# Performance work log

Hardware: AMD Instinct MI355X
Metric: run time of the kernel (lower is better)

## Reference

```python
import jax, jax.numpy as jnp
import numpy as np

HIDDEN = 1024
NUM_TOTAL = 8
NUM_SHARED = 2
NUM_ROUTED = NUM_TOTAL - NUM_SHARED
TOP_K = 2
TOKENS = 16384
SCALE = 0.02


def setup_inputs() -> dict:
    key = jax.random.key(0)
    ks = jax.random.split(key, 12)
    h = HIDDEN
    inp = {
        "x": jax.random.normal(ks[0], (TOKENS, h), dtype=jnp.float32),
        # shared experts: [E_s, in, hidden] / [E_s, hidden] etc. (y = x @ W + b)
        "shared_w1": jax.random.normal(ks[1], (NUM_SHARED, h, h), jnp.float32) * SCALE,
        "shared_b1": jnp.zeros((NUM_SHARED, h), jnp.float32),
        "shared_w2": jax.random.normal(ks[2], (NUM_SHARED, h, h), jnp.float32) * SCALE,
        "shared_b2": jnp.zeros((NUM_SHARED, h), jnp.float32),
        # routed experts
        "routed_w1": jax.random.normal(ks[3], (NUM_ROUTED, h, h), jnp.float32) * SCALE,
        "routed_b1": jnp.zeros((NUM_ROUTED, h), jnp.float32),
        "routed_w2": jax.random.normal(ks[4], (NUM_ROUTED, h, h), jnp.float32) * SCALE,
        "routed_b2": jnp.zeros((NUM_ROUTED, h), jnp.float32),
        # router: Linear(hidden, num_routed)
        "router_w": jax.random.normal(ks[5], (h, NUM_ROUTED), jnp.float32) * SCALE,
        "router_b": jnp.zeros((NUM_ROUTED,), jnp.float32),
    }
    return inp


def _expert_all(x, w1, b1, w2, b2):
    # x: [B, H]; w1/w2: [E, H, H]; returns [B, E, H]
    hmid = jnp.tanh(jnp.einsum("bi,eio->beo", x, w1) + b1)
    return jnp.einsum("beh,eho->beo", hmid, w2) + b2


def reference(x, shared_w1, shared_b1, shared_w2, shared_b2,
              routed_w1, routed_b1, routed_w2, routed_b2,
              router_w, router_b):
    # shared experts: every token through every shared expert, summed
    shared_out = _expert_all(x, shared_w1, shared_b1, shared_w2, shared_b2).sum(axis=1)  # [B,H]

    # router softmax + top-k mask (original weights each expert by
    # routing_weights[:, i] * mask[:, i], i.e. NOT renormalized)
    logits = x @ router_w + router_b                       # [B, E_r]
    routing_weights = jax.nn.softmax(logits, axis=-1)      # [B, E_r]
    _, top_idx = jax.lax.top_k(routing_weights, TOP_K)     # [B, k]
    mask = jax.nn.one_hot(top_idx, NUM_ROUTED, dtype=routing_weights.dtype).sum(axis=1)  # [B, E_r]
    weight = routing_weights * mask                        # [B, E_r]

    # dense all-expert compute masked by top-k (faithful to source loop)
    expert_out = _expert_all(x, routed_w1, routed_b1, routed_w2, routed_b2)  # [B, E_r, H]
    routed_out = jnp.einsum("be,beh->bh", weight, expert_out)

    return shared_out + routed_out
```

## Files before the change

### kernel.cpp

```cpp
#include <hip/hip_runtime.h>
#include <hip/hip_bf16.h>

#define H 1024
#define B_TOK 16384
#define RTILES 262
#define RCAP   (RTILES * 128)

typedef __attribute__((ext_vector_type(8))) short s16x8;
typedef __attribute__((ext_vector_type(4))) float f32x4;

__device__ __forceinline__ short f2bf(float f) {
  __hip_bfloat16 h = __float2bfloat16(f);
  return __builtin_bit_cast(short, h);
}
__device__ __forceinline__ float bf2f(short s) {
  __hip_bfloat16 h = __builtin_bit_cast(__hip_bfloat16, s);
  return __bfloat162float(h);
}

__device__ __forceinline__ void load_lds16(const short* g, short* l) {
  __builtin_amdgcn_global_load_lds((const __attribute__((address_space(1))) void*)g,
                                   (__attribute__((address_space(3))) void*)l,
                                   16, 0, 0);
}

__global__ void cvt_x_k(const float* __restrict__ x, short* __restrict__ xb) {
  const size_t i = ((size_t)blockIdx.x * blockDim.x + threadIdx.x) * 8;
  const float4 a = *(const float4*)(x + i);
  const float4 b = *(const float4*)(x + i + 4);
  s16x8 v;
  v[0] = f2bf(a.x); v[1] = f2bf(a.y); v[2] = f2bf(a.z); v[3] = f2bf(a.w);
  v[4] = f2bf(b.x); v[5] = f2bf(b.y); v[6] = f2bf(b.z); v[7] = f2bf(b.w);
  *(s16x8*)(xb + i) = v;
}

__global__ void transpose_k(const float* __restrict__ sw1, const float* __restrict__ rw1,
                            const float* __restrict__ sw2, const float* __restrict__ rw2,
                            short* __restrict__ w1t, short* __restrict__ w2t_sh,
                            short* __restrict__ w2t_r) {
  __shared__ float tile[64][65];
  const int z = blockIdx.z;
  const float* src;
  short* dst;
  int ldd = H, koff = 0;
  if (z < 8) {
    src = (z < 2) ? sw1 + (size_t)z * H * H : rw1 + (size_t)(z - 2) * H * H;
    dst = w1t + (size_t)z * H * H;
  } else if (z < 10) {
    const int e = z - 8;
    src = sw2 + (size_t)e * H * H;
    dst = w2t_sh; ldd = 2048; koff = e * 1024;
  } else {
    const int e = z - 10;
    src = rw2 + (size_t)e * H * H;
    dst = w2t_r + (size_t)e * H * H;
  }
  const int k0 = blockIdx.y * 64, n0 = blockIdx.x * 64;
  const int t = threadIdx.x;
#pragma unroll
  for (int i = 0; i < 4; ++i) {
    const int kk = (t >> 4) + 16 * i;
    const int nn = (t & 15) * 4;
    const float4 v = *(const float4*)(src + (size_t)(k0 + kk) * H + n0 + nn);
    tile[nn + 0][kk] = v.x; tile[nn + 1][kk] = v.y;
    tile[nn + 2][kk] = v.z; tile[nn + 3][kk] = v.w;
  }
  __syncthreads();
  const int nn = t >> 2;
  const int kk = (t & 3) * 16;
  s16x8 o0, o1;
#pragma unroll
  for (int u = 0; u < 8; ++u) {
    o0[u] = f2bf(tile[nn][kk + u]);
    o1[u] = f2bf(tile[nn][kk + 8 + u]);
  }
  short* drow = dst + (size_t)(n0 + nn) * ldd + koff + k0 + kk;
  *(s16x8*)(drow) = o0;
  *(s16x8*)(drow + 8) = o1;
}

__global__ void logits_k(const float* __restrict__ x, const float* __restrict__ rw,
                         const float* __restrict__ rb, int2* __restrict__ tk) {
  const int lane = threadIdx.x & 63;
  const int b = blockIdx.x * 4 + (threadIdx.x >> 6);
  const float* xr = x + (size_t)b * H;
  float p[6] = {0.f, 0.f, 0.f, 0.f, 0.f, 0.f};
  for (int k = lane; k < H; k += 64) {
    const float xv = xr[k];
    const float* r = rw + k * 6;
#pragma unroll
    for (int e = 0; e < 6; ++e) p[e] += xv * r[e];
  }
#pragma unroll
  for (int e = 0; e < 6; ++e) {
    float v = p[e];
    for (int off = 32; off > 0; off >>= 1) v += __shfl_down(v, off);
    p[e] = v;
  }
  if (lane == 0) {
    float lg[6];
    float mx = -1e30f;
#pragma unroll
    for (int e = 0; e < 6; ++e) { lg[e] = p[e] + rb[e]; mx = fmaxf(mx, lg[e]); }
    float s = 0.f;
#pragma unroll
    for (int e = 0; e < 6; ++e) { lg[e] = __expf(lg[e] - mx); s += lg[e]; }
    const float inv = 1.f / s;
#pragma unroll
    for (int e = 0; e < 6; ++e) lg[e] *= inv;
    int i1 = 0;
#pragma unroll
    for (int e = 1; e < 6; ++e) if (lg[e] > lg[i1]) i1 = e;
    int i2 = (i1 == 0) ? 1 : 0;
#pragma unroll
    for (int e = 0; e < 6; ++e) if (e != i1 && lg[e] > lg[i2]) i2 = e;
    int2 v;
    v.x = i1 | ((int)(unsigned short)f2bf(lg[i1]) << 16);
    v.y = i2 | ((int)(unsigned short)f2bf(lg[i2]) << 16);
    tk[b] = v;
  }
}

__global__ void hist_k(const int2* __restrict__ tk, int* __restrict__ g) {
  __shared__ int h[6];
  const int t = threadIdx.x;
  if (t < 6) h[t] = 0;
  __syncthreads();
  const int2 v = tk[blockIdx.x * 256 + t];
  atomicAdd(&h[v.x & 0xffff], 1);
  atomicAdd(&h[v.y & 0xffff], 1);
  __syncthreads();
  if (t < 6) atomicAdd(&g[t], h[t]);
}

__global__ void prefix_k(int* __restrict__ g) {
  if (threadIdx.x == 0) {
    int run = 0;
#pragma unroll
    for (int e = 0; e < 6; ++e) {
      g[8 + e] = run; g[16 + e] = run;
      run += (g[e] + 127) & ~127;
    }
    g[14] = run;
  }
}

__global__ void scatter_k(const int2* __restrict__ tk, int* __restrict__ g,
                          int* __restrict__ asg) {
  __shared__ int lcnt[6];
  __shared__ int lbase[6];
  const int t = threadIdx.x;
  if (t < 6) lcnt[t] = 0;
  __syncthreads();
  const int tok = blockIdx.x * 256 + t;
  const int2 v = tk[tok];
  const int e1 = v.x & 0xffff, e2 = v.y & 0xffff;
  const int p1 = atomicAdd(&lcnt[e1], 1);
  const int p2 = atomicAdd(&lcnt[e2], 1);
  __syncthreads();
  if (t < 6) lbase[t] = atomicAdd(&g[16 + t], lcnt[t]);
  __syncthreads();
  asg[lbase[e1] + p1] = tok | (v.x & 0xffff0000);
  asg[lbase[e2] + p2] = tok | (v.y & 0xffff0000);
}

__device__ __forceinline__ void gemm_core64(const short* __restrict__ A, int lda,
                                            const short* __restrict__ Bt, int ldb, int K,
                                            short* smem, int m0, int n0,
                                            const int* __restrict__ asg, int acap,
                                            f32x4 acc[4][4]) {
  const int tid = threadIdx.x, lane = tid & 63, w = tid >> 6;
  const int q8 = (lane >> 4) * 8, r16 = lane & 15;
  const int wr = w >> 1, wc = w & 1;

  const short* gp[4];
#pragma unroll
  for (int ii = 0; ii < 4; ++ii) {
    const int c2 = w * 4 + ii;
    if (c2 < 8) {
      int slot = m0 + c2 * 16 + r16;
      int gr;
      if (asg) {
        int tv = asg[slot] & 0xffff;
        gr = tv < B_TOK ? tv : B_TOK - 1;
      } else {
        gr = slot < acap ? slot : acap - 1;
      }
      gp[ii] = A + (size_t)gr * lda + q8;
    } else {
      gp[ii] = Bt + (size_t)(n0 + (c2 - 8) * 16 + r16) * ldb + q8;
    }
  }
  short* lbase = smem + w * 4096;

  for (int k0 = 0; k0 < K; k0 += 64) {
    __syncthreads();
#pragma unroll
    for (int i = 0; i < 8; ++i)
      load_lds16(gp[i >> 1] + k0 + (i & 1) * 32, lbase + i * 512);
    __syncthreads();
#pragma unroll
    for (int s = 0; s < 2; ++s) {
      s16x8 af[4], bfv[4];
#pragma unroll
      for (int i = 0; i < 4; ++i)
        af[i] = *(const s16x8*)(smem + ((wr * 4 + i) * 2 + s) * 512 + lane * 8);
#pragma unroll
      for (int j = 0; j < 4; ++j)
        bfv[j] = *(const s16x8*)(smem + (16 + (wc * 4 + j) * 2 + s) * 512 + lane * 8);
#pragma unroll
      for (int i = 0; i < 4; ++i)
#pragma unroll
        for (int j = 0; j < 4; ++j)
          acc[i][j] = __builtin_amdgcn_mfma_f32_16x16x32_bf16(af[i], bfv[j], acc[i][j], 0, 0, 0);
    }
  }
}

template <int ROUTED>
__global__ __launch_bounds__(256) void gemm1_k(const short* __restrict__ A, int lda,
                                               const short* __restrict__ W1, int ldb, int K,
                                               const float* __restrict__ b1,
                                               short* __restrict__ Out, int ldo,
                                               const int* __restrict__ asg,
                                               const int* __restrict__ g, int rowcap) {
  const int m0 = blockIdx.x * 128, n0 = blockIdx.y * 128;
  const short* Bt = W1;
  const float* bias = b1;
  if (ROUTED) {
    if (m0 >= g[14]) return;
    int e = 0;
#pragma unroll
    for (int j = 1; j < 6; ++j) if (m0 >= g[8 + j]) e = j;
    Bt = W1 + (size_t)e * H * H;
    bias = b1 + (size_t)e * H;
  }
  __shared__ __align__(16) short smem[16384];
  f32x4 acc[4][4];
#pragma unroll
  for (int i = 0; i < 4; ++i)
#pragma unroll
    for (int j = 0; j < 4; ++j) acc[i][j] = (f32x4){0.f, 0.f, 0.f, 0.f};
  gemm_core64(A, lda, Bt, ldb, K, smem, m0, n0, ROUTED ? asg : nullptr, 1 << 30, acc);

  const int tid = threadIdx.x, lane = tid & 63, w = tid >> 6;
  const int wr = w >> 1, wc = w & 1, q = lane >> 4, c16 = lane & 15;
  __syncthreads();
#pragma unroll
  for (int j = 0; j < 4; ++j) {
    const int colL = wc * 64 + j * 16 + c16;
    const float bv = bias[n0 + colL];
#pragma unroll
    for (int i = 0; i < 4; ++i)
#pragma unroll
      for (int r = 0; r < 4; ++r)
        smem[(wr * 64 + i * 16 + q * 4 + r) * 128 + colL] = f2bf(tanhf(acc[i][j][r] + bv));
  }
  __syncthreads();
#pragma unroll
  for (int p = 0; p < 8; ++p) {
    const int rowL = p * 16 + (tid >> 4);
    const int colL = (tid & 15) * 8;
    const int gr = m0 + rowL;
    if (gr < rowcap)
      *(s16x8*)(Out + (size_t)gr * ldo + n0 + colL) = *(const s16x8*)(smem + rowL * 128 + colL);
  }
}

template <int MODE>
__global__ __launch_bounds__(256) void gemm2_k(const short* __restrict__ A, int lda,
                                               const short* __restrict__ W2, int ldb, int K,
                                               const float* __restrict__ b2a,
                                               const float* __restrict__ b2b,
                                               float* __restrict__ Out,
                                               const int* __restrict__ asg,
                                               const int* __restrict__ g, int acap) {
  const int m0 = blockIdx.x * 128, n0 = blockIdx.y * 128;
  const short* Bt = W2;
  const float* bias = b2a;
  if (MODE == 3) {
    if (m0 >= g[14]) return;
    int e = 0;
#pragma unroll
    for (int j = 1; j < 6; ++j) if (m0 >= g[8 + j]) e = j;
    Bt = W2 + (size_t)e * H * H;
    bias = b2a + (size_t)e * H;
  }
  __shared__ __align__(16) short smem[16384];
  f32x4 acc[4][4];
#pragma unroll
  for (int i = 0; i < 4; ++i)
#pragma unroll
    for (int j = 0; j < 4; ++j) acc[i][j] = (f32x4){0.f, 0.f, 0.f, 0.f};
  gemm_core64(A, lda, Bt, ldb, K, smem, m0, n0, nullptr, acap, acc);

  const int tid = threadIdx.x, lane = tid & 63, w = tid >> 6;
  const int wr = w >> 1, wc = w & 1, q = lane >> 4, c16 = lane & 15;

  if (MODE == 0) {
    float* cs = (float*)smem;
    __syncthreads();
#pragma unroll
    for (int half = 0; half < 2; ++half) {
      if (wr == half) {
#pragma unroll
        for (int j = 0; j < 4; ++j) {
          const int colL = wc * 64 + j * 16 + c16;
          const float bv = b2a[n0 + colL] + b2b[n0 + colL];
#pragma unroll
          for (int i = 0; i < 4; ++i)
#pragma unroll
            for (int r = 0; r < 4; ++r)
              cs[(i * 16 + q * 4 + r) * 128 + colL] = acc[i][j][r] + bv;
        }
      }
      __syncthreads();
#pragma unroll
      for (int p = 0; p < 8; ++p) {
        const int rowL = p * 8 + (tid >> 5);
        const int colL = (tid & 31) * 4;
        *(float4*)(Out + (size_t)(m0 + half * 64 + rowL) * H + n0 + colL) =
            *(const float4*)(cs + rowL * 128 + colL);
      }
      __syncthreads();
    }
  } else {
    const int mb = m0 + wr * 64, nb = n0 + wc * 64;
#pragma unroll
    for (int i = 0; i < 4; ++i) {
      int av[4];
#pragma unroll
      for (int r = 0; r < 4; ++r) av[r] = asg[mb + i * 16 + q * 4 + r];
#pragma unroll
      for (int j = 0; j < 4; ++j) {
        const int col = nb + j * 16 + c16;
        const float bv = bias[col];
#pragma unroll
        for (int r = 0; r < 4; ++r) {
          if (av[r] == -1) continue;
          const int tok = av[r] & 0xffff;
          const float wt = bf2f((short)((unsigned)av[r] >> 16));
          atomicAdd(&Out[(size_t)tok * H + col], (acc[i][j][r] + bv) * wt);
        }
      }
    }
  }
}

extern "C" void kernel_launch(void* const* d_in, const int* in_sizes, int n_in,
                              void* d_out, int out_size, void* d_ws, size_t ws_size,
                              hipStream_t stream) {
  const float* x        = (const float*)d_in[0];
  const float* sw1      = (const float*)d_in[1];
  const float* sb1      = (const float*)d_in[2];
  const float* sw2      = (const float*)d_in[3];
  const float* sb2      = (const float*)d_in[4];
  const float* rw1      = (const float*)d_in[5];
  const float* rb1      = (const float*)d_in[6];
  const float* rw2      = (const float*)d_in[7];
  const float* rb2      = (const float*)d_in[8];
  const float* router_w = (const float*)d_in[9];
  const float* router_b = (const float*)d_in[10];
  float* out = (float*)d_out;

  char* ws = (char*)d_ws;
  short* xb     = (short*)(ws);
  short* w1t    = (short*)(ws + (size_t)33554432);
  short* w2t_r  = (short*)(ws + (size_t)50331648);
  short* w2t_sh = (short*)(ws + (size_t)62914560);
  short* hm_sh  = (short*)(ws + (size_t)67108864);
  short* hm_r   = (short*)(ws + (size_t)62914560);
  int2*  tk     = (int2*)hm_sh;
  int*   g      = (int*)(ws + (size_t)134217728);
  int*   asg    = (int*)(ws + (size_t)134217984);

  hipMemsetAsync(g, 0, 64, stream);
  hipMemsetAsync(asg, 0xFF, RCAP * sizeof(int), stream);

  cvt_x_k<<<8192, 256, 0, stream>>>(x, xb);
  transpose_k<<<dim3(16, 16, 16), 256, 0, stream>>>(sw1, rw1, sw2, rw2, w1t, w2t_sh, w2t_r);
  logits_k<<<4096, 256, 0, stream>>>(x, router_w, router_b, tk);
  hist_k<<<64, 256, 0, stream>>>(tk, g);
  prefix_k<<<1, 64, 0, stream>>>(g);
  scatter_k<<<64, 256, 0, stream>>>(tk, g, asg);

  gemm1_k<0><<<dim3(128, 16), 256, 0, stream>>>(xb, H, w1t, H, H, sb1, hm_sh, 2048,
                                                nullptr, nullptr, 1 << 30);
  gemm2_k<0><<<dim3(128, 8), 256, 0, stream>>>(hm_sh, 2048, w2t_sh, 2048, 2048,
                                               sb2, sb2 + H, out, nullptr, nullptr, 1 << 30);

  gemm1_k<1><<<dim3(RTILES, 8), 256, 0, stream>>>(xb, H, w1t + (size_t)2 * H * H, H, H,
                                                  rb1, hm_r, H, asg, g, RCAP);
  gemm2_k<3><<<dim3(RTILES, 8), 256, 0, stream>>>(hm_r, H, w2t_r, H, H,
                                                  rb2, nullptr, out, asg, g, RCAP);
}
```

Measured before the change: 834.1 us.

## Remap GEMM tiles across XCDs, use fast tanh, raise occupancy hint

The GEMM grids become one-dimensional and each block index is remapped so that consecutive tiles land on the same XCD (an 8-way chiplet-aware swizzle), which should improve L2 reuse of A rows and weight columns. Row-major tile ordering within an XCD keeps N tiles of one M stripe together. The tanh epilogue switches from tanhf to an exp/fast-divide formula. Launch bounds now request 6 waves per SIMD, which may force register spilling. The fast tanh is less accurate and can produce NaN for large inputs when exp overflows to inf, though 2/inf gives 0, so it should stay safe.

```diff
diff --git a/kernel.cpp b/kernel.cpp
--- a/kernel.cpp
+++ b/kernel.cpp
@@ -18,10 +18,25 @@
   return __bfloat162float(h);
 }
 
+__device__ __forceinline__ float fast_tanh(float x) {
+  const float e = __expf(2.f * x);
+  return 1.f - __fdividef(2.f, e + 1.f);
+}
+
 __device__ __forceinline__ void load_lds16(const short* g, short* l) {
   __builtin_amdgcn_global_load_lds((const __attribute__((address_space(1))) void*)g,
                                    (__attribute__((address_space(3))) void*)l,
                                    16, 0, 0);
+}
+
+template <int NY>
+__device__ __forceinline__ void tile_coords128(int& m0, int& n0) {
+  const int nwg = gridDim.x, o = blockIdx.x;
+  const int q = nwg >> 3, r = nwg & 7;
+  const int x = o & 7, oo = o >> 3;
+  const int wg = (x < r ? x * (q + 1) : r * (q + 1) + (x - r) * q) + oo;
+  m0 = (wg / NY) * 128;
+  n0 = (wg % NY) * 128;
 }
 
 __global__ void cvt_x_k(const float* __restrict__ x, short* __restrict__ xb) {
@@ -217,14 +232,15 @@
   }
 }
 
-template <int ROUTED>
-__global__ __launch_bounds__(256) void gemm1_k(const short* __restrict__ A, int lda,
-                                               const short* __restrict__ W1, int ldb, int K,
-                                               const float* __restrict__ b1,
-                                               short* __restrict__ Out, int ldo,
-                                               const int* __restrict__ asg,
-                                               const int* __restrict__ g, int rowcap) {
-  const int m0 = blockIdx.x * 128, n0 = blockIdx.y * 128;
+template <int ROUTED, int NY>
+__global__ __launch_bounds__(256, 6) void gemm1_k(const short* __restrict__ A, int lda,
+                                                  const short* __restrict__ W1, int ldb, int K,
+                                                  const float* __restrict__ b1,
+                                                  short* __restrict__ Out, int ldo,
+                                                  const int* __restrict__ asg,
+                                                  const int* __restrict__ g, int rowcap) {
+  int m0, n0;
+  tile_coords128<NY>(m0, n0);
   const short* Bt = W1;
   const float* bias = b1;
   if (ROUTED) {
@@ -254,7 +270,7 @@
     for (int i = 0; i < 4; ++i)
 #pragma unroll
       for (int r = 0; r < 4; ++r)
-        smem[(wr * 64 + i * 16 + q * 4 + r) * 128 + colL] = f2bf(tanhf(acc[i][j][r] + bv));
+        smem[(wr * 64 + i * 16 + q * 4 + r) * 128 + colL] = f2bf(fast_tanh(acc[i][j][r] + bv));
   }
   __syncthreads();
 #pragma unroll
@@ -267,15 +283,16 @@
   }
 }
 
-template <int MODE>
-__global__ __launch_bounds__(256) void gemm2_k(const short* __restrict__ A, int lda,
-                                               const short* __restrict__ W2, int ldb, int K,
-                                               const float* __restrict__ b2a,
-                                               const float* __restrict__ b2b,
-                                               float* __restrict__ Out,
-                                               const int* __restrict__ asg,
-                                               const int* __restrict__ g, int acap) {
-  const int m0 = blockIdx.x * 128, n0 = blockIdx.y * 128;
+template <int MODE, int NY>
+__global__ __launch_bounds__(256, 6) void gemm2_k(const short* __restrict__ A, int lda,
+                                                  const short* __restrict__ W2, int ldb, int K,
+                                                  const float* __restrict__ b2a,
+                                                  const float* __restrict__ b2b,
+                                                  float* __restrict__ Out,
+                                                  const int* __restrict__ asg,
+                                                  const int* __restrict__ g, int acap) {
+  int m0, n0;
+  tile_coords128<NY>(m0, n0);
   const short* Bt = W2;
   const float* bias = b2a;
   if (MODE == 3) {
@@ -384,13 +401,13 @@
   prefix_k<<<1, 64, 0, stream>>>(g);
   scatter_k<<<64, 256, 0, stream>>>(tk, g, asg);
 
-  gemm1_k<0><<<dim3(128, 16), 256, 0, stream>>>(xb, H, w1t, H, H, sb1, hm_sh, 2048,
-                                                nullptr, nullptr, 1 << 30);
-  gemm2_k<0><<<dim3(128, 8), 256, 0, stream>>>(hm_sh, 2048, w2t_sh, 2048, 2048,
-                                               sb2, sb2 + H, out, nullptr, nullptr, 1 << 30);
-
-  gemm1_k<1><<<dim3(RTILES, 8), 256, 0, stream>>>(xb, H, w1t + (size_t)2 * H * H, H, H,
-                                                  rb1, hm_r, H, asg, g, RCAP);
-  gemm2_k<3><<<dim3(RTILES, 8), 256, 0, stream>>>(hm_r, H, w2t_r, H, H,
-                                                  rb2, nullptr, out, asg, g, RCAP);
-}
+  gemm1_k<0, 16><<<128 * 16, 256, 0, stream>>>(xb, H, w1t, H, H, sb1, hm_sh, 2048,
+                                               nullptr, nullptr, 1 << 30);
+  gemm2_k<0, 8><<<128 * 8, 256, 0, stream>>>(hm_sh, 2048, w2t_sh, 2048, 2048,
+                                             sb2, sb2 + H, out, nullptr, nullptr, 1 << 30);
+
+  gemm1_k<1, 8><<<RTILES * 8, 256, 0, stream>>>(xb, H, w1t + (size_t)2 * H * H, H, H,
+                                                rb1, hm_r, H, asg, g, RCAP);
+  gemm2_k<3, 8><<<RTILES * 8, 256, 0, stream>>>(hm_r, H, w2t_r, H, H,
+                                                rb2, nullptr, out, asg, g, RCAP);
+}
```

New measurement: 812.5 us. 2.6% less time.
